# Kernel optimization log

Measured on AMD Instinct MI355X. Metric: run time of the kernel, lower is better.

Reference implementation:

```python
import jax, jax.numpy as jnp
import numpy as np
from jax.scipy.linalg import expm

B, T = 32, 4096
FREQ_DIM = 128
HID = 64
OUT_DIM = 2
N_COMP = 4
DT = 0.1
EPS = 1e-5


def setup_inputs() -> dict:
    key = jax.random.key(0)
    ks = jax.random.split(key, 16)
    f32 = jnp.float32

    def lin(k, out_d, in_d):
        bound = 1.0 / np.sqrt(in_d)
        kw, kb = jax.random.split(k)
        W = jax.random.uniform(kw, (out_d, in_d), f32, -bound, bound)
        b = jax.random.uniform(kb, (out_d,), f32, -bound, bound)
        return W, b

    x = jax.random.normal(ks[0], (B, T, 1), f32)
    # EnhancedWavePhysics params
    freq_spectrum = jnp.linspace(1.0, 20.0, FREQ_DIM, dtype=f32)
    pm_w1, pm_b1 = lin(ks[1], 128, 1)
    pm_w2, pm_b2 = lin(ks[2], FREQ_DIM * 2, 128)
    wc_w, wc_b = lin(ks[3], HID, FREQ_DIM)
    amp_ctrl = jnp.ones((1,), f32) * 0.1
    # quantum encoder
    qe_w1, qe_b1 = lin(ks[4], HID * 2, HID)
    qe_w2, qe_b2 = lin(ks[5], HID * 4, HID * 2)
    # layernorm
    ln_g = jnp.ones((HID * 4,), f32)
    ln_b = jnp.zeros((HID * 4,), f32)
    # skew-symmetric hamiltonians [4, 64, 64]
    A = jax.random.normal(ks[6], (N_COMP, HID, HID), f32) * 0.05
    hams = (A - jnp.swapaxes(A, -1, -2)) / 2.0
    # interference net
    int_w1, int_b1 = lin(ks[7], 32, 4)
    int_w2, int_b2 = lin(ks[8], OUT_DIM, 32)
    int_strength = jnp.ones((1,), f32)
    return dict(x=x, freq_spectrum=freq_spectrum, pm_w1=pm_w1, pm_b1=pm_b1,
                pm_w2=pm_w2, pm_b2=pm_b2, wc_w=wc_w, wc_b=wc_b,
                amp_ctrl=amp_ctrl, qe_w1=qe_w1, qe_b1=qe_b1, qe_w2=qe_w2,
                qe_b2=qe_b2, ln_g=ln_g, ln_b=ln_b, hams=hams,
                int_w1=int_w1, int_b1=int_b1, int_w2=int_w2, int_b2=int_b2,
                int_strength=int_strength)


def reference(x, freq_spectrum, pm_w1, pm_b1, pm_w2, pm_b2, wc_w, wc_b,
              amp_ctrl, qe_w1, qe_b1, qe_w2, qe_b2, ln_g, ln_b, hams,
              int_w1, int_b1, int_w2, int_b2, int_strength):
    Bx, Tx, _ = x.shape
    # --- EnhancedWavePhysics ---
    mod = jnp.tanh(x @ pm_w1.T + pm_b1) @ pm_w2.T + pm_b2            # [B,T,2F]
    amplitude, phase = jnp.split(mod, 2, axis=-1)                     # [B,T,F]
    amplitude = jnp.tanh(amplitude) * amp_ctrl
    time = jnp.linspace(0.0, 2.0 * np.pi, Tx)[None, :, None]          # [1,T,1]
    freqs = freq_spectrum[None, None, :]                              # [1,1,F]
    wave_components = amplitude * jnp.sin(freqs * time + phase)       # [B,T,F]
    wave_field = jnp.tanh(wave_components @ wc_w.T + wc_b)            # [B,T,H]
    # --- quantum encoder + layernorm ---
    q = jnp.tanh(wave_field @ qe_w1.T + qe_b1) @ qe_w2.T + qe_b2      # [B,T,4H]
    mu = q.mean(-1, keepdims=True)
    var = q.var(-1, keepdims=True)
    q = (q - mu) / jnp.sqrt(var + EPS) * ln_g + ln_b
    psi = q.reshape(Bx, Tx, N_COMP, HID)                              # [B,T,C,D]
    # --- Hamiltonian evolution: torch does matrix_exp(-1j*(1j*H)*dt)=expm(H*dt)
    #     (H skew-symmetric real => U real orthogonal), then psi @ U.T, take real.
    U = jax.vmap(expm)(hams * DT)                                     # [C,D,D]
    evolved = jnp.einsum('btcd,ced->btce', psi, U)                    # [B,T,C,D]
    # --- EnhancedInterference ---
    spec = jnp.abs(jnp.fft.fft(evolved, axis=1))                      # [B,T,C,D]
    freq_w = jax.nn.softmax(spec.mean(-1), axis=1)                    # [B,T,C]
    weighted = jnp.sum(spec * freq_w[..., None], axis=1)              # [B,C,D]
    spatial_avg = weighted.mean(-1)                                   # [B,C]
    out = jnp.tanh(spatial_avg @ int_w1.T + int_b1) @ int_w2.T + int_b2
    return out * int_strength                                         # [B,out_dim]
```

## Files before the change

### kernel.cpp

```cpp
#include <hip/hip_runtime.h>
#include <hip/hip_bf16.h>

#define TT 4096
#define BB 32

typedef unsigned short ushort_t;
typedef __attribute__((ext_vector_type(8))) short short8v;
typedef __attribute__((ext_vector_type(4))) float float4v;

__device__ inline ushort_t bf16rn(float v) {
    unsigned u = __float_as_uint(v);
    unsigned r = (u + 0x7FFFu + ((u >> 16) & 1u)) >> 16;
    return (ushort_t)r;
}
__device__ inline float bf16tof(ushort_t h) {
    return __uint_as_float(((unsigned)h) << 16);
}
__device__ inline int SW(int i) { return i + (i >> 5); }

__device__ inline float fast_tanh(float x) {
    float e = __builtin_amdgcn_exp2f(x * 2.8853900817779268f);
    return 1.0f - 2.0f * __builtin_amdgcn_rcpf(e + 1.0f);
}
__device__ inline float fast_sin(float x) {
    return __builtin_amdgcn_sinf(x * 0.15915494309189535f);
}

__global__ __launch_bounds__(256) void k1_expm(const float* __restrict__ hams,
                                               float* __restrict__ U)
{
    int c = blockIdx.x, tid = threadIdx.x;
    __shared__ float M[4096], P[4096], Acc[4096];
    const float* H = hams + c * 4096;
    for (int k = tid; k < 4096; k += 256) {
        float m = H[k] * 0.1f;
        M[k] = m; P[k] = m;
        Acc[k] = m + (((k >> 6) == (k & 63)) ? 1.0f : 0.0f);
    }
    __syncthreads();
    int j = tid & 63;
    float mcol[64];
    #pragma unroll
    for (int k = 0; k < 64; k++) mcol[k] = M[k * 64 + j];
    for (int term = 2; term <= 8; term++) {
        float inv = 1.0f / (float)term;
        float np_[16];
        #pragma unroll
        for (int r = 0; r < 16; r++) {
            int i = (tid >> 6) + 4 * r;
            float a = 0.f;
            #pragma unroll
            for (int k = 0; k < 64; k++) a = fmaf(P[i * 64 + k], mcol[k], a);
            np_[r] = a * inv;
        }
        __syncthreads();
        #pragma unroll
        for (int r = 0; r < 16; r++) {
            int i = (tid >> 6) + 4 * r;
            P[i * 64 + j] = np_[r];
            Acc[i * 64 + j] += np_[r];
        }
        __syncthreads();
    }
    for (int k = tid; k < 4096; k += 256) U[c * 4096 + k] = Acc[k];
}

__global__ void split_all(const float* __restrict__ pw2, const float* __restrict__ wcw,
                          const float* __restrict__ qw1, const float* __restrict__ qw2,
                          ushort_t* __restrict__ wb)
{
    int i = blockIdx.x * 256 + threadIdx.x;
    const float* src; ushort_t *hi, *lo; int off;
    if (i < 32768)      { src = pw2; hi = wb;          lo = wb + 32768;  off = i; }
    else if (i < 40960) { src = wcw; hi = wb + 65536;  lo = wb + 73728;  off = i - 32768; }
    else if (i < 49152) { src = qw1; hi = wb + 81920;  lo = wb + 90112;  off = i - 40960; }
    else                { src = qw2; hi = wb + 98304;  lo = wb + 131072; off = i - 49152; }
    float v = src[off];
    ushort_t h = bf16rn(v);
    hi[off] = h;
    lo[off] = bf16rn(v - bf16tof(h));
}

__global__ __launch_bounds__(256, 2) void gemm_s1(
    const ushort_t* __restrict__ Whi, const ushort_t* __restrict__ Wlo,
    const float* __restrict__ bias,
    const float* __restrict__ x, const float* __restrict__ pw1,
    const float* __restrict__ pb1,
    const float* __restrict__ freq, const float* __restrict__ ampc,
    ushort_t* __restrict__ O)
{
    __shared__ ushort_t OT[2][2048];
    int tid = threadIdx.x;
    int w = tid >> 6, l = tid & 63, l15 = l & 15, kg = l >> 4;
    int kofb = kg * 8;

    short8v bh[4][4], bl[4][4];
    #pragma unroll
    for (int i = 0; i < 4; i++) {
        int n = (w + 4 * i) * 16 + l15;
        #pragma unroll
        for (int kc = 0; kc < 4; kc++) {
            int kof = kc * 32 + kofb;
            bh[i][kc] = *(const short8v*)(Whi + (size_t)n * 128 + kof);
            bl[i][kc] = *(const short8v*)(Wlo + (size_t)n * 128 + kof);
        }
    }
    float am = ampc[0];
    float fr[2], ba[2], bp[2];
    #pragma unroll
    for (int i = 0; i < 2; i++) {
        int f = (w + 4 * i) * 16 + l15;
        fr[i] = freq[f]; ba[i] = bias[f]; bp[i] = bias[128 + f];
    }

    int mbase = blockIdx.x * 64;
    for (int mi = 0; mi < 4; mi++) {
        int m0 = mbase + mi * 16;
        float xv = x[m0 + l15];
        short8v ah[4], al[4];
        #pragma unroll
        for (int kc = 0; kc < 4; kc++) {
            int k0 = kc * 32 + kofb;
            float4 w0 = *(const float4*)(pw1 + k0);
            float4 w1v = *(const float4*)(pw1 + k0 + 4);
            float4 b0 = *(const float4*)(pb1 + k0);
            float4 b1v = *(const float4*)(pb1 + k0 + 4);
            #pragma unroll
            for (int j = 0; j < 8; j++) {
                float wj = (j < 4) ? (&w0.x)[j] : (&w1v.x)[j - 4];
                float bj = (j < 4) ? (&b0.x)[j] : (&b1v.x)[j - 4];
                float v = fast_tanh(fmaf(xv, wj, bj));
                ushort_t h = bf16rn(v);
                ah[kc][j] = (short)h;
                al[kc][j] = (short)bf16rn(v - bf16tof(h));
            }
        }
        float4v acc[4];
        #pragma unroll
        for (int i = 0; i < 4; i++) acc[i] = (float4v){0.f, 0.f, 0.f, 0.f};
        #pragma unroll
        for (int kc = 0; kc < 4; kc++) {
            #pragma unroll
            for (int i = 0; i < 4; i++) {
                acc[i] = __builtin_amdgcn_mfma_f32_16x16x32_bf16(ah[kc], bh[i][kc], acc[i], 0, 0, 0);
                acc[i] = __builtin_amdgcn_mfma_f32_16x16x32_bf16(ah[kc], bl[i][kc], acc[i], 0, 0, 0);
                acc[i] = __builtin_amdgcn_mfma_f32_16x16x32_bf16(al[kc], bh[i][kc], acc[i], 0, 0, 0);
            }
        }
        int buf = mi & 1;
        #pragma unroll
        for (int i = 0; i < 2; i++) {
            int f = (w + 4 * i) * 16 + l15;
            #pragma unroll
            for (int r = 0; r < 4; r++) {
                int m = m0 + kg * 4 + r;
                float timev = 6.283185307179586f * (float)(m & 4095) / 4095.0f;
                float a = fast_tanh(acc[i][r] + ba[i]) * am;
                float ph = acc[i + 2][r] + bp[i];
                float v = a * fast_sin(fmaf(fr[i], timev, ph));
                OT[buf][(kg * 4 + r) * 128 + f] = bf16rn(v);
            }
        }
        __syncthreads();
        *(uint4*)(O + (size_t)m0 * 128 + tid * 8) = *(const uint4*)(&OT[buf][tid * 8]);
    }
}

__global__ __launch_bounds__(256, 2) void s23_v2(
    const ushort_t* __restrict__ A,
    const ushort_t* __restrict__ W2hi, const ushort_t* __restrict__ W2lo,
    const float* __restrict__ b2,
    const ushort_t* __restrict__ W3hi, const ushort_t* __restrict__ W3lo,
    const float* __restrict__ b3,
    ushort_t* __restrict__ OHi, ushort_t* __restrict__ OLo)
{
    __shared__ unsigned WF[2][16][65];
    __shared__ ushort_t OThi[2][2048], OTlo[2][2048];
    int tid = threadIdx.x;
    int w = tid >> 6, l = tid & 63, l15 = l & 15, kg = l >> 4;
    int kofb = kg * 8;

    short8v w2h[4], w2l[4];
    #pragma unroll
    for (int kc = 0; kc < 4; kc++) {
        int n = w * 16 + l15;
        int kof = kc * 32 + kofb;
        w2h[kc] = *(const short8v*)(W2hi + (size_t)n * 128 + kof);
        w2l[kc] = *(const short8v*)(W2lo + (size_t)n * 128 + kof);
    }
    short8v w3h[2][2], w3l[2][2];
    #pragma unroll
    for (int i = 0; i < 2; i++) {
        int n = (w + 4 * i) * 16 + l15;
        #pragma unroll
        for (int kc = 0; kc < 2; kc++) {
            int kof = kc * 32 + kofb;
            w3h[i][kc] = *(const short8v*)(W3hi + (size_t)n * 64 + kof);
            w3l[i][kc] = *(const short8v*)(W3lo + (size_t)n * 64 + kof);
        }
    }
    float b2v = b2[w * 16 + l15];
    float b3v[2];
    #pragma unroll
    for (int i = 0; i < 2; i++) b3v[i] = b3[(w + 4 * i) * 16 + l15];

    int mbase = blockIdx.x * 64;
    for (int mi = 0; mi < 4; mi++) {
        int m0 = mbase + mi * 16;
        short8v ah[4];
        #pragma unroll
        for (int kc = 0; kc < 4; kc++) {
            int kof = kc * 32 + kofb;
            ah[kc] = *(const short8v*)(A + (size_t)(m0 + l15) * 128 + kof);
        }
        float4v acc1 = (float4v){0.f, 0.f, 0.f, 0.f};
        #pragma unroll
        for (int kc = 0; kc < 4; kc++) {
            acc1 = __builtin_amdgcn_mfma_f32_16x16x32_bf16(ah[kc], w2h[kc], acc1, 0, 0, 0);
            acc1 = __builtin_amdgcn_mfma_f32_16x16x32_bf16(ah[kc], w2l[kc], acc1, 0, 0, 0);
        }
        int buf = mi & 1;
        #pragma unroll
        for (int r = 0; r < 4; r++) {
            float v = fast_tanh(acc1[r] + b2v);
            ushort_t h = bf16rn(v);
            ushort_t lo2 = bf16rn(v - bf16tof(h));
            WF[buf][kg * 4 + r][w * 16 + l15] = (unsigned)h | ((unsigned)lo2 << 16);
        }
        __syncthreads();
        float4v acc2[2];
        acc2[0] = (float4v){0.f, 0.f, 0.f, 0.f};
        acc2[1] = (float4v){0.f, 0.f, 0.f, 0.f};
        #pragma unroll
        for (int kc = 0; kc < 2; kc++) {
            short8v a2h, a2l;
            #pragma unroll
            for (int j = 0; j < 8; j++) {
                unsigned u = WF[buf][l15][kc * 32 + kofb + j];
                a2h[j] = (short)(u & 0xFFFFu);
                a2l[j] = (short)(u >> 16);
            }
            #pragma unroll
            for (int i = 0; i < 2; i++) {
                acc2[i] = __builtin_amdgcn_mfma_f32_16x16x32_bf16(a2h, w3h[i][kc], acc2[i], 0, 0, 0);
                acc2[i] = __builtin_amdgcn_mfma_f32_16x16x32_bf16(a2h, w3l[i][kc], acc2[i], 0, 0, 0);
                acc2[i] = __builtin_amdgcn_mfma_f32_16x16x32_bf16(a2l, w3h[i][kc], acc2[i], 0, 0, 0);
            }
        }
        #pragma unroll
        for (int i = 0; i < 2; i++) {
            int n = (w + 4 * i) * 16 + l15;
            #pragma unroll
            for (int r = 0; r < 4; r++) {
                float v = fast_tanh(acc2[i][r] + b3v[i]);
                ushort_t h = bf16rn(v);
                OThi[buf][(kg * 4 + r) * 128 + n] = h;
                OTlo[buf][(kg * 4 + r) * 128 + n] = bf16rn(v - bf16tof(h));
            }
        }
        __syncthreads();
        *(uint4*)(OHi + (size_t)m0 * 128 + tid * 8) = *(const uint4*)(&OThi[buf][tid * 8]);
        *(uint4*)(OLo + (size_t)m0 * 128 + tid * 8) = *(const uint4*)(&OTlo[buf][tid * 8]);
    }
}

__global__ __launch_bounds__(256, 2) void gemm_s4(
    const ushort_t* __restrict__ Ahi, const ushort_t* __restrict__ Alo,
    const ushort_t* __restrict__ Whi, const ushort_t* __restrict__ Wlo,
    const float* __restrict__ bias,
    const float* __restrict__ lng, const float* __restrict__ lnb,
    unsigned* __restrict__ psiu)
{
    __shared__ float partS[2][4][16], partSS[2][4][16];
    __shared__ unsigned PT[256 * 65];
    int tid = threadIdx.x;
    int w = tid >> 6, l = tid & 63, l15 = l & 15, kg = l >> 4;
    int kofb = kg * 8;

    short8v bh[4][4], bl[4][4];
    #pragma unroll
    for (int i = 0; i < 4; i++) {
        int n = (w + 4 * i) * 16 + l15;
        #pragma unroll
        for (int kc = 0; kc < 4; kc++) {
            int kof = kc * 32 + kofb;
            bh[i][kc] = *(const short8v*)(Whi + (size_t)n * 128 + kof);
            bl[i][kc] = *(const short8v*)(Wlo + (size_t)n * 128 + kof);
        }
    }
    float bv[4], g4[4], be4[4];
    #pragma unroll
    for (int i = 0; i < 4; i++) {
        int n = (w + 4 * i) * 16 + l15;
        bv[i] = bias[n]; g4[i] = lng[n]; be4[i] = lnb[n];
    }

    int mbase = blockIdx.x * 64;
    int b = mbase >> 12, tbase = mbase & 4095;
    for (int mi = 0; mi < 4; mi++) {
        int m0 = mbase + mi * 16;
        short8v ah[4], al[4];
        #pragma unroll
        for (int kc = 0; kc < 4; kc++) {
            int kof = kc * 32 + kofb;
            ah[kc] = *(const short8v*)(Ahi + (size_t)(m0 + l15) * 128 + kof);
            al[kc] = *(const short8v*)(Alo + (size_t)(m0 + l15) * 128 + kof);
        }
        float4v acc[4];
        #pragma unroll
        for (int i = 0; i < 4; i++) acc[i] = (float4v){0.f, 0.f, 0.f, 0.f};
        #pragma unroll
        for (int kc = 0; kc < 4; kc++) {
            #pragma unroll
            for (int i = 0; i < 4; i++) {
                acc[i] = __builtin_amdgcn_mfma_f32_16x16x32_bf16(ah[kc], bh[i][kc], acc[i], 0, 0, 0);
                acc[i] = __builtin_amdgcn_mfma_f32_16x16x32_bf16(ah[kc], bl[i][kc], acc[i], 0, 0, 0);
                acc[i] = __builtin_amdgcn_mfma_f32_16x16x32_bf16(al[kc], bh[i][kc], acc[i], 0, 0, 0);
            }
        }
        float s[4] = {0, 0, 0, 0}, ss[4] = {0, 0, 0, 0};
        #pragma unroll
        for (int i = 0; i < 4; i++) {
            #pragma unroll
            for (int r = 0; r < 4; r++) {
                float v = acc[i][r] + bv[i];
                s[r] += v; ss[r] += v * v;
            }
        }
        #pragma unroll
        for (int r = 0; r < 4; r++) {
            #pragma unroll
            for (int off = 1; off < 16; off <<= 1) {
                s[r] += __shfl_xor(s[r], off);
                ss[r] += __shfl_xor(ss[r], off);
            }
        }
        int pb_ = mi & 1;
        if (l15 == 0) {
            #pragma unroll
            for (int r = 0; r < 4; r++) {
                partS[pb_][w][kg * 4 + r] = s[r];
                partSS[pb_][w][kg * 4 + r] = ss[r];
            }
        }
        __syncthreads();
        float mu[4], rstd[4];
        #pragma unroll
        for (int r = 0; r < 4; r++) {
            float ts = 0.f, tss = 0.f;
            #pragma unroll
            for (int wv = 0; wv < 4; wv++) {
                ts += partS[pb_][wv][kg * 4 + r];
                tss += partSS[pb_][wv][kg * 4 + r];
            }
            mu[r] = ts * (1.0f / 256.0f);
            float var = tss * (1.0f / 256.0f) - mu[r] * mu[r];
            rstd[r] = rsqrtf(var + 1e-5f);
        }
        #pragma unroll
        for (int i = 0; i < 4; i++) {
            int n = (w + 4 * i) * 16 + l15;
            #pragma unroll
            for (int r = 0; r < 4; r++) {
                float v = (acc[i][r] + bv[i] - mu[r]) * rstd[r] * g4[i] + be4[i];
                ushort_t h = bf16rn(v);
                ushort_t lo2 = bf16rn(v - bf16tof(h));
                PT[n * 65 + mi * 16 + kg * 4 + r] = (unsigned)h | ((unsigned)lo2 << 16);
            }
        }
    }
    __syncthreads();
    int n = tid;
    size_t gb = ((size_t)(b * 256 + n)) * 4096 + tbase;
    #pragma unroll
    for (int j = 0; j < 16; j++) {
        uint4 v;
        v.x = PT[n * 65 + j * 4 + 0];
        v.y = PT[n * 65 + j * 4 + 1];
        v.z = PT[n * 65 + j * 4 + 2];
        v.w = PT[n * 65 + j * 4 + 3];
        *(uint4*)(psiu + gb + j * 4) = v;
    }
}

__global__ __launch_bounds__(256) void k3a_mfma(float* __restrict__ psi,
                                                const float* __restrict__ U)
{
    __shared__ unsigned QP[64 * 261];
    int bid = blockIdx.x;
    int b = bid >> 6, c = (bid >> 4) & 3, tc = bid & 15;
    int t0 = tc * 256;
    int tid = threadIdx.x;
    int w = tid >> 6, l = tid & 63;
    int l15 = l & 15, kq = l >> 4;
    size_t gbase = ((size_t)(b * 256 + c * 64)) * TT + t0;
    const unsigned* psiu = (const unsigned*)psi;

    for (int i = 0; i < 16; i++) {
        int r_ = i * 4 + w;
        int t4 = l * 4;
        uint4 v = *(const uint4*)(psiu + gbase + (size_t)r_ * TT + t4);
        QP[r_ * 261 + t4 + 0] = v.x;
        QP[r_ * 261 + t4 + 1] = v.y;
        QP[r_ * 261 + t4 + 2] = v.z;
        QP[r_ * 261 + t4 + 3] = v.w;
    }
    __syncthreads();

    short8v ua_hi[2], ua_lo[2];
    #pragma unroll
    for (int kc = 0; kc < 2; kc++) {
        #pragma unroll
        for (int j = 0; j < 8; j++) {
            float v = U[c * 4096 + (w * 16 + l15) * 64 + kc * 32 + kq * 8 + j];
            ushort_t h = bf16rn(v);
            ua_hi[kc][j] = (short)h;
            ua_lo[kc][j] = (short)bf16rn(v - bf16tof(h));
        }
    }

    for (int nt = 0; nt < 16; nt++) {
        float4v acc = (float4v){0.f, 0.f, 0.f, 0.f};
        #pragma unroll
        for (int kc = 0; kc < 2; kc++) {
            short8v b_hi, b_lo;
            #pragma unroll
            for (int j = 0; j < 8; j++) {
                unsigned u = QP[(kc * 32 + kq * 8 + j) * 261 + nt * 16 + l15];
                b_hi[j] = (short)(u & 0xFFFFu);
                b_lo[j] = (short)(u >> 16);
            }
            acc = __builtin_amdgcn_mfma_f32_16x16x32_bf16(ua_hi[kc], b_hi, acc, 0, 0, 0);
            acc = __builtin_amdgcn_mfma_f32_16x16x32_bf16(ua_hi[kc], b_lo, acc, 0, 0, 0);
            acc = __builtin_amdgcn_mfma_f32_16x16x32_bf16(ua_lo[kc], b_hi, acc, 0, 0, 0);
        }
        #pragma unroll
        for (int r = 0; r < 4; r++) {
            int e = w * 16 + kq * 4 + r;
            psi[gbase + (size_t)e * TT + nt * 16 + l15] = acc[r];
        }
    }
}

__global__ __launch_bounds__(256, 2) void k3b_fft(const float* __restrict__ ev,
                                                  float* __restrict__ msum8)
{
    __shared__ float re[4224], im[4224];
    int b = blockIdx.x, c = blockIdx.y, g = blockIdx.z;
    int tid = threadIdx.x;

    float macc[8];
    #pragma unroll
    for (int r = 0; r < 8; r++) macc[r] = 0.f;
    float macc8 = 0.f;

    size_t base = (((size_t)b * 4 + c) * 64 + (size_t)g * 8) * TT;
    for (int p = 0; p < 4; p++) {
        __syncthreads();
        for (int r = 0; r < 4; r++) {
            int t0 = (r * 256 + tid) * 4;
            float4 va = *(const float4*)(ev + base + (size_t)(2 * p) * TT + t0);
            float4 vb = *(const float4*)(ev + base + (size_t)(2 * p + 1) * TT + t0);
            #pragma unroll
            for (int j = 0; j < 4; j++) {
                int rv = __brev((unsigned)(t0 + j)) >> 20;
                re[SW(rv)] = (&va.x)[j];
                im[SW(rv)] = (&vb.x)[j];
            }
        }
        __syncthreads();

        #pragma unroll
        for (int trip = 0; trip < 3; trip++) {
            const int sh = trip * 4;
            int pos = tid & ((1 << sh) - 1);
            int grp = tid >> sh;
            int i0 = (grp << (sh + 4)) + pos;

            float yr[16], yi[16];
            #pragma unroll
            for (int j = 0; j < 16; j++) {
                int a = SW(i0 + (j << sh));
                yr[j] = re[a]; yi[j] = im[a];
            }
            float ang = -(float)pos / (float)(16 << sh);
            float t1r = __builtin_amdgcn_cosf(ang);
            float t1i = __builtin_amdgcn_sinf(ang);
            float t2r = t1r * t1r - t1i * t1i, t2i = 2.f * t1r * t1i;
            float t4r = t2r * t2r - t2i * t2i, t4i = 2.f * t2r * t2i;
            float t8r = t4r * t4r - t4i * t4i, t8i = 2.f * t4r * t4i;

            #pragma unroll
            for (int m = 0; m < 8; m++) {
                int j0 = 2 * m, j1 = j0 + 1;
                float tr = t8r * yr[j1] - t8i * yi[j1];
                float ti = t8r * yi[j1] + t8i * yr[j1];
                yr[j1] = yr[j0] - tr; yi[j1] = yi[j0] - ti;
                yr[j0] += tr;         yi[j0] += ti;
            }
            #pragma unroll
            for (int bs = 0; bs < 16; bs += 4) {
                {
                    int j0 = bs, j1 = bs + 2;
                    float tr = t4r * yr[j1] - t4i * yi[j1];
                    float ti = t4r * yi[j1] + t4i * yr[j1];
                    yr[j1] = yr[j0] - tr; yi[j1] = yi[j0] - ti;
                    yr[j0] += tr;         yi[j0] += ti;
                }
                {
                    int j0 = bs + 1, j1 = bs + 3;
                    float tr = t4i * yr[j1] + t4r * yi[j1];
                    float ti = t4i * yi[j1] - t4r * yr[j1];
                    yr[j1] = yr[j0] - tr; yi[j1] = yi[j0] - ti;
                    yr[j0] += tr;         yi[j0] += ti;
                }
            }
            {
                float wr = t2r, wi = t2i;
                #pragma unroll
                for (int j = 0; j < 4; j++) {
                    #pragma unroll
                    for (int bs = 0; bs < 16; bs += 8) {
                        int j0 = bs + j, j1 = j0 + 4;
                        float tr = wr * yr[j1] - wi * yi[j1];
                        float ti = wr * yi[j1] + wi * yr[j1];
                        yr[j1] = yr[j0] - tr; yi[j1] = yi[j0] - ti;
                        yr[j0] += tr;         yi[j0] += ti;
                    }
                    float nwr = (wr + wi) * 0.70710678f;
                    float nwi = (wi - wr) * 0.70710678f;
                    wr = nwr; wi = nwi;
                }
            }
            {
                float wr = t1r, wi = t1i;
                #pragma unroll
                for (int j = 0; j < 8; j++) {
                    int j0 = j, j1 = j + 8;
                    float tr = wr * yr[j1] - wi * yi[j1];
                    float ti = wr * yi[j1] + wi * yr[j1];
                    yr[j1] = yr[j0] - tr; yi[j1] = yi[j0] - ti;
                    yr[j0] += tr;         yi[j0] += ti;
                    float nwr = wr * 0.92387953f + wi * 0.38268343f;
                    float nwi = wi * 0.92387953f - wr * 0.38268343f;
                    wr = nwr; wi = nwi;
                }
            }
            #pragma unroll
            for (int j = 0; j < 16; j++) {
                int a = SW(i0 + (j << sh));
                re[a] = yr[j]; im[a] = yi[j];
            }
            __syncthreads();
        }

        for (int r = 0; r < 8; r++) {
            int k = tid + r * 256;
            int mk = (4096 - k) & 4095;
            float rk = re[SW(k)], ik = im[SW(k)];
            float rm = re[SW(mk)], imm = im[SW(mk)];
            float dA1 = rk + rm, dA2 = ik - imm;
            float dB1 = ik + imm, dB2 = rk - rm;
            float magA = 0.5f * sqrtf(dA1 * dA1 + dA2 * dA2);
            float magB = 0.5f * sqrtf(dB1 * dB1 + dB2 * dB2);
            macc[r] += magA + magB;
        }
        if (tid == 0) {
            float rk = re[SW(2048)], ik = im[SW(2048)];
            macc8 += fabsf(rk) + fabsf(ik);
        }
    }
    float* ms = msum8 + (((size_t)b * 4 + c) * 8 + g) * 4096;
    for (int r = 0; r < 8; r++) {
        int k = tid + r * 256;
        ms[k] = macc[r];
        if (k > 0) ms[4096 - k] = macc[r];
    }
    if (tid == 0) ms[2048] = macc8;
}

__global__ __launch_bounds__(256) void k4_softdot(const float* __restrict__ msum8,
                                                  float* __restrict__ sa)
{
    __shared__ float m[4096];
    __shared__ float red[256];
    int bc = blockIdx.x, tid = threadIdx.x;
    const float* ms = msum8 + (size_t)bc * 8 * 4096;
    float lmax = -1e30f;
    for (int k = tid; k < 4096; k += 256) {
        float v = 0.f;
        #pragma unroll
        for (int g = 0; g < 8; g++) v += ms[g * 4096 + k];
        v *= (1.0f / 64.0f);
        m[k] = v;
        lmax = fmaxf(lmax, v);
    }
    red[tid] = lmax; __syncthreads();
    for (int s2 = 128; s2 > 0; s2 >>= 1) {
        if (tid < s2) red[tid] = fmaxf(red[tid], red[tid + s2]);
        __syncthreads();
    }
    float mx = red[0]; __syncthreads();
    float lsum = 0.f, ldot = 0.f;
    for (int k = tid; k < 4096; k += 256) {
        float e = expf(m[k] - mx);
        lsum += e; ldot += e * m[k];
    }
    red[tid] = lsum; __syncthreads();
    for (int s2 = 128; s2 > 0; s2 >>= 1) {
        if (tid < s2) red[tid] += red[tid + s2];
        __syncthreads();
    }
    float tsum = red[0]; __syncthreads();
    red[tid] = ldot; __syncthreads();
    for (int s2 = 128; s2 > 0; s2 >>= 1) {
        if (tid < s2) red[tid] += red[tid + s2];
        __syncthreads();
    }
    if (tid == 0) sa[bc] = red[0] / tsum;
}

__global__ void k5_head(const float* __restrict__ sa,
                        const float* __restrict__ w1, const float* __restrict__ b1,
                        const float* __restrict__ w2, const float* __restrict__ b2,
                        const float* __restrict__ strength,
                        float* __restrict__ out)
{
    int b = threadIdx.x;
    if (b >= 32) return;
    float s0 = sa[b * 4 + 0], s1 = sa[b * 4 + 1];
    float s2 = sa[b * 4 + 2], s3 = sa[b * 4 + 3];
    float h[32];
    #pragma unroll
    for (int j = 0; j < 32; j++)
        h[j] = tanhf(b1[j] + w1[j * 4 + 0] * s0 + w1[j * 4 + 1] * s1 +
                     w1[j * 4 + 2] * s2 + w1[j * 4 + 3] * s3);
    float st = strength[0];
    #pragma unroll
    for (int o = 0; o < 2; o++) {
        float a = b2[o];
        #pragma unroll
        for (int j = 0; j < 32; j++) a = fmaf(w2[o * 32 + j], h[j], a);
        out[b * 2 + o] = a * st;
    }
}

extern "C" void kernel_launch(void* const* d_in, const int* in_sizes, int n_in,
                              void* d_out, int out_size, void* d_ws, size_t ws_size,
                              hipStream_t stream)
{
    const float* x    = (const float*)d_in[0];
    const float* freq = (const float*)d_in[1];
    const float* pw1  = (const float*)d_in[2];
    const float* pb1  = (const float*)d_in[3];
    const float* pw2  = (const float*)d_in[4];
    const float* pb2  = (const float*)d_in[5];
    const float* wcw  = (const float*)d_in[6];
    const float* wcb  = (const float*)d_in[7];
    const float* ampc = (const float*)d_in[8];
    const float* qw1  = (const float*)d_in[9];
    const float* qb1  = (const float*)d_in[10];
    const float* qw2  = (const float*)d_in[11];
    const float* qb2  = (const float*)d_in[12];
    const float* lng  = (const float*)d_in[13];
    const float* lnb  = (const float*)d_in[14];
    const float* hams = (const float*)d_in[15];
    const float* iw1  = (const float*)d_in[16];
    const float* ib1  = (const float*)d_in[17];
    const float* iw2  = (const float*)d_in[18];
    const float* ib2  = (const float*)d_in[19];
    const float* istr = (const float*)d_in[20];

    char* wsb = (char*)d_ws;
    ushort_t* AHi = (ushort_t*)(wsb + 0);
    ushort_t* ALo = (ushort_t*)(wsb + 33554432);
    ushort_t* Bwcf = (ushort_t*)(wsb + 67108864);
    float*    psi = (float*)(wsb + 67108864);
    float*    msum8 = (float*)(wsb + 0);
    float*    U    = (float*)(wsb + 201326592);
    float*    sa   = (float*)(wsb + 201392128);
    ushort_t* wb   = (ushort_t*)(wsb + 203489792);
    ushort_t *pw2hi = wb,          *pw2lo = wb + 32768;
    ushort_t *wcwhi = wb + 65536,  *wcwlo = wb + 73728;
    ushort_t *qw1hi = wb + 81920,  *qw1lo = wb + 90112;
    ushort_t *qw2hi = wb + 98304,  *qw2lo = wb + 131072;
    float* out = (float*)d_out;

    k1_expm<<<4, 256, 0, stream>>>(hams, U);
    split_all<<<320, 256, 0, stream>>>(pw2, wcw, qw1, qw2, wb);

    gemm_s1<<<2048, 256, 0, stream>>>(pw2hi, pw2lo, pb2, x, pw1, pb1,
                                      freq, ampc, Bwcf);
    s23_v2<<<2048, 256, 0, stream>>>(Bwcf, wcwhi, wcwlo, wcb,
        qw1hi, qw1lo, qb1, AHi, ALo);
    gemm_s4<<<2048, 256, 0, stream>>>(AHi, ALo, qw2hi, qw2lo, qb2,
        lng, lnb, (unsigned*)psi);

    k3a_mfma<<<2048, 256, 0, stream>>>(psi, U);
    k3b_fft<<<dim3(32, 4, 8), 256, 0, stream>>>(psi, msum8);
    k4_softdot<<<128, 256, 0, stream>>>(msum8, sa);
    k5_head<<<1, 64, 0, stream>>>(sa, iw1, ib1, iw2, ib2, istr, out);
}
```

Measured before the change: 365.6 us.

## Fuse Hamiltonian evolution into layernorm GEMM and store evolved psi as bf16 pairs

```diff
diff --git a/kernel.cpp b/kernel.cpp
--- a/kernel.cpp
+++ b/kernel.cpp
@@ -264,15 +264,16 @@
     }
 }
 
-__global__ __launch_bounds__(256, 2) void gemm_s4(
+__global__ __launch_bounds__(256, 2) void gemm_s4e(
     const ushort_t* __restrict__ Ahi, const ushort_t* __restrict__ Alo,
     const ushort_t* __restrict__ Whi, const ushort_t* __restrict__ Wlo,
     const float* __restrict__ bias,
     const float* __restrict__ lng, const float* __restrict__ lnb,
+    const float* __restrict__ U,
     unsigned* __restrict__ psiu)
 {
     __shared__ float partS[2][4][16], partSS[2][4][16];
-    __shared__ unsigned PT[256 * 65];
+    __shared__ unsigned PT[256 * 33];
     int tid = threadIdx.x;
     int w = tid >> 6, l = tid & 63, l15 = l & 15, kg = l >> 4;
     int kofb = kg * 8;
@@ -295,9 +296,9 @@
         bv[i] = bias[n]; g4[i] = lng[n]; be4[i] = lnb[n];
     }
 
-    int mbase = blockIdx.x * 64;
+    int mbase = blockIdx.x * 32;
     int b = mbase >> 12, tbase = mbase & 4095;
-    for (int mi = 0; mi < 4; mi++) {
+    for (int mi = 0; mi < 2; mi++) {
         int m0 = mbase + mi * 16;
         short8v ah[4], al[4];
         #pragma unroll
@@ -365,84 +366,56 @@
                 float v = (acc[i][r] + bv[i] - mu[r]) * rstd[r] * g4[i] + be4[i];
                 ushort_t h = bf16rn(v);
                 ushort_t lo2 = bf16rn(v - bf16tof(h));
-                PT[n * 65 + mi * 16 + kg * 4 + r] = (unsigned)h | ((unsigned)lo2 << 16);
+                PT[n * 33 + mi * 16 + kg * 4 + r] = (unsigned)h | ((unsigned)lo2 << 16);
             }
         }
     }
     __syncthreads();
-    int n = tid;
-    size_t gb = ((size_t)(b * 256 + n)) * 4096 + tbase;
-    #pragma unroll
-    for (int j = 0; j < 16; j++) {
-        uint4 v;
-        v.x = PT[n * 65 + j * 4 + 0];
-        v.y = PT[n * 65 + j * 4 + 1];
-        v.z = PT[n * 65 + j * 4 + 2];
-        v.w = PT[n * 65 + j * 4 + 3];
-        *(uint4*)(psiu + gb + j * 4) = v;
-    }
-}
-
-__global__ __launch_bounds__(256) void k3a_mfma(float* __restrict__ psi,
-                                                const float* __restrict__ U)
-{
-    __shared__ unsigned QP[64 * 261];
-    int bid = blockIdx.x;
-    int b = bid >> 6, c = (bid >> 4) & 3, tc = bid & 15;
-    int t0 = tc * 256;
-    int tid = threadIdx.x;
-    int w = tid >> 6, l = tid & 63;
-    int l15 = l & 15, kq = l >> 4;
-    size_t gbase = ((size_t)(b * 256 + c * 64)) * TT + t0;
-    const unsigned* psiu = (const unsigned*)psi;
-
-    for (int i = 0; i < 16; i++) {
-        int r_ = i * 4 + w;
-        int t4 = l * 4;
-        uint4 v = *(const uint4*)(psiu + gbase + (size_t)r_ * TT + t4);
-        QP[r_ * 261 + t4 + 0] = v.x;
-        QP[r_ * 261 + t4 + 1] = v.y;
-        QP[r_ * 261 + t4 + 2] = v.z;
-        QP[r_ * 261 + t4 + 3] = v.w;
-    }
-    __syncthreads();
-
-    short8v ua_hi[2], ua_lo[2];
-    #pragma unroll
-    for (int kc = 0; kc < 2; kc++) {
-        #pragma unroll
-        for (int j = 0; j < 8; j++) {
-            float v = U[c * 4096 + (w * 16 + l15) * 64 + kc * 32 + kq * 8 + j];
-            ushort_t h = bf16rn(v);
-            ua_hi[kc][j] = (short)h;
-            ua_lo[kc][j] = (short)bf16rn(v - bf16tof(h));
-        }
-    }
-
-    for (int nt = 0; nt < 16; nt++) {
-        float4v acc = (float4v){0.f, 0.f, 0.f, 0.f};
+
+    int c = w;
+    size_t gb = ((size_t)(b * 256 + c * 64)) * 4096 + tbase;
+    for (int et = 0; et < 4; et++) {
+        short8v ua_h[2], ua_l[2];
         #pragma unroll
         for (int kc = 0; kc < 2; kc++) {
-            short8v b_hi, b_lo;
             #pragma unroll
             for (int j = 0; j < 8; j++) {
-                unsigned u = QP[(kc * 32 + kq * 8 + j) * 261 + nt * 16 + l15];
-                b_hi[j] = (short)(u & 0xFFFFu);
-                b_lo[j] = (short)(u >> 16);
-            }
-            acc = __builtin_amdgcn_mfma_f32_16x16x32_bf16(ua_hi[kc], b_hi, acc, 0, 0, 0);
-            acc = __builtin_amdgcn_mfma_f32_16x16x32_bf16(ua_hi[kc], b_lo, acc, 0, 0, 0);
-            acc = __builtin_amdgcn_mfma_f32_16x16x32_bf16(ua_lo[kc], b_hi, acc, 0, 0, 0);
-        }
-        #pragma unroll
-        for (int r = 0; r < 4; r++) {
-            int e = w * 16 + kq * 4 + r;
-            psi[gbase + (size_t)e * TT + nt * 16 + l15] = acc[r];
-        }
-    }
-}
-
-__global__ __launch_bounds__(256, 2) void k3b_fft(const float* __restrict__ ev,
+                float v = U[c * 4096 + (et * 16 + l15) * 64 + kc * 32 + kofb + j];
+                ushort_t h = bf16rn(v);
+                ua_h[kc][j] = (short)h;
+                ua_l[kc][j] = (short)bf16rn(v - bf16tof(h));
+            }
+        }
+        #pragma unroll
+        for (int tt = 0; tt < 2; tt++) {
+            float4v acc = (float4v){0.f, 0.f, 0.f, 0.f};
+            #pragma unroll
+            for (int kc = 0; kc < 2; kc++) {
+                short8v b_h, b_l;
+                #pragma unroll
+                for (int j = 0; j < 8; j++) {
+                    unsigned u = PT[(c * 64 + kc * 32 + kofb + j) * 33 + tt * 16 + l15];
+                    b_h[j] = (short)(u & 0xFFFFu);
+                    b_l[j] = (short)(u >> 16);
+                }
+                acc = __builtin_amdgcn_mfma_f32_16x16x32_bf16(ua_h[kc], b_h, acc, 0, 0, 0);
+                acc = __builtin_amdgcn_mfma_f32_16x16x32_bf16(ua_h[kc], b_l, acc, 0, 0, 0);
+                acc = __builtin_amdgcn_mfma_f32_16x16x32_bf16(ua_l[kc], b_h, acc, 0, 0, 0);
+            }
+            #pragma unroll
+            for (int r = 0; r < 4; r++) {
+                int e = et * 16 + kg * 4 + r;
+                float v = acc[r];
+                ushort_t h = bf16rn(v);
+                ushort_t lo2 = bf16rn(v - bf16tof(h));
+                psiu[gb + (size_t)e * 4096 + tt * 16 + l15] =
+                    (unsigned)h | ((unsigned)lo2 << 16);
+            }
+        }
+    }
+}
+
+__global__ __launch_bounds__(256, 2) void k3b_fft(const unsigned* __restrict__ ev,
                                                   float* __restrict__ msum8)
 {
     __shared__ float re[4224], im[4224];
@@ -459,13 +432,14 @@
         __syncthreads();
         for (int r = 0; r < 4; r++) {
             int t0 = (r * 256 + tid) * 4;
-            float4 va = *(const float4*)(ev + base + (size_t)(2 * p) * TT + t0);
-            float4 vb = *(const float4*)(ev + base + (size_t)(2 * p + 1) * TT + t0);
+            uint4 va = *(const uint4*)(ev + base + (size_t)(2 * p) * TT + t0);
+            uint4 vb = *(const uint4*)(ev + base + (size_t)(2 * p + 1) * TT + t0);
             #pragma unroll
             for (int j = 0; j < 4; j++) {
                 int rv = __brev((unsigned)(t0 + j)) >> 20;
-                re[SW(rv)] = (&va.x)[j];
-                im[SW(rv)] = (&vb.x)[j];
+                unsigned ua = (&va.x)[j], ub = (&vb.x)[j];
+                re[SW(rv)] = bf16tof((ushort_t)(ua & 0xFFFFu)) + bf16tof((ushort_t)(ua >> 16));
+                im[SW(rv)] = bf16tof((ushort_t)(ub & 0xFFFFu)) + bf16tof((ushort_t)(ub >> 16));
             }
         }
         __syncthreads();
@@ -675,7 +649,7 @@
     ushort_t* AHi = (ushort_t*)(wsb + 0);
     ushort_t* ALo = (ushort_t*)(wsb + 33554432);
     ushort_t* Bwcf = (ushort_t*)(wsb + 67108864);
-    float*    psi = (float*)(wsb + 67108864);
+    unsigned* psi = (unsigned*)(wsb + 67108864);
     float*    msum8 = (float*)(wsb + 0);
     float*    U    = (float*)(wsb + 201326592);
     float*    sa   = (float*)(wsb + 201392128);
@@ -693,10 +667,9 @@
                                       freq, ampc, Bwcf);
     s23_v2<<<2048, 256, 0, stream>>>(Bwcf, wcwhi, wcwlo, wcb,
         qw1hi, qw1lo, qb1, AHi, ALo);
-    gemm_s4<<<2048, 256, 0, stream>>>(AHi, ALo, qw2hi, qw2lo, qb2,
-        lng, lnb, (unsigned*)psi);
-
-    k3a_mfma<<<2048, 256, 0, stream>>>(psi, U);
+    gemm_s4e<<<4096, 256, 0, stream>>>(AHi, ALo, qw2hi, qw2lo, qb2,
+        lng, lnb, U, psi);
+
     k3b_fft<<<dim3(32, 4, 8), 256, 0, stream>>>(psi, msum8);
     k4_softdot<<<128, 256, 0, stream>>>(msum8, sa);
     k5_head<<<1, 64, 0, stream>>>(sa, iw1, ib1, iw2, ib2, istr, out);
```

New measurement: 352.1 us. 3.7% less time.
